# Optimization experiments

Measured on AMD Instinct MI355X. Metric: run time of the kernel, lower is better.

The kernel has to match this reference:

```python
import jax, jax.numpy as jnp
import numpy as np

# config
B, V, S, D = 2, 8, 256, 2048
NH, NKV, KVR = 32, 8, 2
HD = D // NH            # 64
G = NH // NKV           # GQA group size = 4
INIT = 0.02


def _neighbor_idx():
    # replicates generate_neighbor: left neighbors (i-half..i-1) then right (i+1..i+half), circular
    half = KVR // 2
    offsets = np.concatenate([np.arange(-half, 0), np.arange(1, half + 1)])
    return (np.arange(V)[:, None] + offsets[None, :]) % V  # [V, KVR]


def setup_inputs() -> dict:
    key = jax.random.key(0)
    k1, k2, k3, k4 = jax.random.split(key, 4)
    x = jax.random.normal(k1, (B, V, S, D), jnp.float32)
    wq = jax.random.normal(k2, (D, NH * HD), jnp.float32) * INIT
    wkv = jax.random.normal(k3, (D, 2 * NKV * HD), jnp.float32) * INIT
    wo = jax.random.normal(k4, (D, D), jnp.float32) * INIT
    return {"x": x, "wq": wq, "wkv": wkv, "wo": wo}


def reference(x, wq, wkv, wo):
    b, v, s, d = x.shape
    idx = _neighbor_idx()  # [V, KVR] static

    # Q projection: [b, v, s, NH*HD]
    xq = (x @ wq).reshape(b, v, s, NKV, G, HD)  # grouped-query layout (kv head, group)

    # neighbor gather: [b, v, KVR, s, d] -> [b, v, KVR*s, d]
    x_kv = x[:, idx].reshape(b, v, KVR * s, d)
    kv = x_kv @ wkv
    xk, xv = jnp.split(kv, 2, axis=-1)
    xk = xk.reshape(b, v, KVR * s, NKV, HD)
    xv = xv.reshape(b, v, KVR * s, NKV, HD)

    # grouped-query SDPA (no mask, eval mode): avoids materializing repeated K/V
    scale = 1.0 / jnp.sqrt(jnp.asarray(HD, x.dtype))
    scores = jnp.einsum('bvsngh,bvtnh->bvngst', xq, xk) * scale  # [b,v,NKV,G,s,KVR*s]
    attn = jax.nn.softmax(scores, axis=-1)
    out = jnp.einsum('bvngst,bvtnh->bvsngh', attn, xv).reshape(b, v, s, d)
    return out @ wo
```

## Files before the change

kernel.cpp:

```cpp
#include <hip/hip_runtime.h>
#include <stdint.h>

typedef unsigned short u16;
typedef unsigned int   u32;
typedef short short8 __attribute__((ext_vector_type(8)));
typedef float f32x4  __attribute__((ext_vector_type(4)));

__device__ __forceinline__ u16 f2bf(float f){
  u32 u = __builtin_bit_cast(u32, f);
  u32 r = (u + 0x7FFFu + ((u >> 16) & 1u)) >> 16;
  return (u16)r;
}
__device__ __forceinline__ u32 packbf(float a, float b){
  return (u32)f2bf(a) | ((u32)f2bf(b) << 16);
}
__device__ __forceinline__ void gload16(const u16* g, u16* l){
  __builtin_amdgcn_global_load_lds((const __attribute__((address_space(1))) void*)g,
                                   (__attribute__((address_space(3))) void*)l, 16, 0, 0);
}

__global__ __launch_bounds__(256) void k_cvt_bf16(const float* __restrict__ x,
                                                  u16* __restrict__ y, int n8){
  int i = blockIdx.x * 256 + threadIdx.x;
  if (i >= n8) return;
  const float4* p = (const float4*)x + (size_t)i * 2;
  float4 a = p[0], b = p[1];
  short8 o;
  o[0] = f2bf(a.x); o[1] = f2bf(a.y); o[2] = f2bf(a.z); o[3] = f2bf(a.w);
  o[4] = f2bf(b.x); o[5] = f2bf(b.y); o[6] = f2bf(b.z); o[7] = f2bf(b.w);
  *(short8*)(y + (size_t)i * 8) = o;
}

__global__ __launch_bounds__(256) void k_transpose_w(const float* __restrict__ in,
                                                     u16* __restrict__ out, int R, int C){
  __shared__ float tile[32][33];
  int nc = C >> 5;
  int cb = blockIdx.x % nc, rb = blockIdx.x / nc;
  int tx = threadIdx.x & 31, ty = threadIdx.x >> 5;
#pragma unroll
  for (int i = 0; i < 4; ++i){
    int r = rb * 32 + ty + i * 8;
    tile[ty + i * 8][tx] = in[(size_t)r * C + cb * 32 + tx];
  }
  __syncthreads();
#pragma unroll
  for (int i = 0; i < 4; ++i){
    int c = cb * 32 + ty + i * 8;
    out[(size_t)c * R + rb * 32 + tx] = f2bf(tile[tx][ty + i * 8]);
  }
}

template<int BN, int NFRAG, int BLOADS, typename CT>
__global__ __launch_bounds__(512, 2) void k_gemm8p(const u16* __restrict__ A,
                                                   const u16* __restrict__ Bt,
                                                   CT* __restrict__ C,
                                                   int N, int K){
  constexpr int SZA = 256 * 128;
  constexpr int SZB = BN * 128;
  constexpr int SZ  = SZA + SZB;
  constexpr int WT_N = BN / 4;
  __shared__ char lds[2 * SZ];

  int tid = threadIdx.x, lane = tid & 63, wid = tid >> 6;
  int l16 = lane & 15, g4 = lane >> 4;
  int wm = wid >> 2, wn = wid & 3;
  int bid = blockIdx.x;
  int wg = (bid & 7) * 32 + (bid >> 3);
  int bm = wg >> 4, bn = wg & 15;

  const u16* baseA = A  + (size_t)(bm * 256) * K;
  const u16* baseB = Bt + (size_t)(bn * BN) * K;

  int aLds[4], aG[4];
#pragma unroll
  for (int i = 0; i < 4; ++i){
    int q = (wid * 4 + i) * 1024 + lane * 16;
    int row = q >> 7, c = q & 127;
    int cs = c ^ ((row & 7) << 4);
    aLds[i] = q; aG[i] = row * K + (cs >> 1);
  }
  int bLds[BLOADS], bG[BLOADS];
#pragma unroll
  for (int j = 0; j < BLOADS; ++j){
    int q = (wid * BLOADS + j) * 1024 + lane * 16;
    int row = q >> 7, c = q & 127;
    int cs = c ^ ((row & 7) << 4);
    bLds[j] = q; bG[j] = row * K + (cs >> 1);
  }
  auto stageA = [&](int t){
    char* dst = lds + (t & 1) * SZ;
#pragma unroll
    for (int i = 0; i < 4; ++i) gload16(baseA + aG[i] + t * 64, (u16*)(dst + aLds[i]));
  };
  auto stageB = [&](int t){
    char* dst = lds + (t & 1) * SZ + SZA;
#pragma unroll
    for (int j = 0; j < BLOADS; ++j) gload16(baseB + bG[j] + t * 64, (u16*)(dst + bLds[j]));
  };
  auto rdA = [&](const char* Ab, int m, int ks){
    int row = wm * 128 + m * 16 + l16;
    return *(const short8*)(Ab + row * 128 + ((ks * 64 + g4 * 16) ^ ((row & 7) << 4)));
  };
  auto rdB = [&](const char* Bb, int nf, int ks){
    int row = wn * WT_N + nf * 16 + l16;
    return *(const short8*)(Bb + row * 128 + ((ks * 64 + g4 * 16) ^ ((row & 7) << 4)));
  };

  f32x4 zero4 = {0.f, 0.f, 0.f, 0.f};
  f32x4 acc[8][NFRAG];
#pragma unroll
  for (int i = 0; i < 8; ++i)
#pragma unroll
    for (int j = 0; j < NFRAG; ++j) acc[i][j] = zero4;

  int NK = K >> 6;
  stageA(0); stageB(0);
  asm volatile("s_waitcnt vmcnt(0)" ::: "memory");

  for (int kt = 0; kt < NK; ++kt){
    const char* Ab = lds + (kt & 1) * SZ;
    const char* Bb = Ab + SZA;
    bool st = (kt + 1 < NK);
    __builtin_amdgcn_s_barrier();
    short8 bf0[NFRAG], a0[4], a1[4], bf1[NFRAG], a2[4], a3[4];
#pragma unroll
    for (int nf = 0; nf < NFRAG; ++nf) bf0[nf] = rdB(Bb, nf, 0);
#pragma unroll
    for (int m = 0; m < 4; ++m) a0[m] = rdA(Ab, m, 0);
    if (st) stageA(kt + 1);
#pragma unroll
    for (int m = 0; m < 4; ++m) a1[m] = rdA(Ab, 4 + m, 0);
    __builtin_amdgcn_s_setprio(1);
#pragma unroll
    for (int m = 0; m < 4; ++m)
#pragma unroll
      for (int nf = 0; nf < NFRAG; ++nf)
        acc[m][nf] = __builtin_amdgcn_mfma_f32_16x16x32_bf16(a0[m], bf0[nf], acc[m][nf], 0, 0, 0);
    __builtin_amdgcn_s_setprio(0);
    __builtin_amdgcn_s_barrier();
    if (st) stageB(kt + 1);
#pragma unroll
    for (int nf = 0; nf < NFRAG; ++nf) bf1[nf] = rdB(Bb, nf, 1);
#pragma unroll
    for (int m = 0; m < 4; ++m) a2[m] = rdA(Ab, m, 1);
    __builtin_amdgcn_s_setprio(1);
#pragma unroll
    for (int m = 0; m < 4; ++m)
#pragma unroll
      for (int nf = 0; nf < NFRAG; ++nf)
        acc[4 + m][nf] = __builtin_amdgcn_mfma_f32_16x16x32_bf16(a1[m], bf0[nf], acc[4 + m][nf], 0, 0, 0);
    __builtin_amdgcn_s_setprio(0);
    __builtin_amdgcn_s_barrier();
#pragma unroll
    for (int m = 0; m < 4; ++m) a3[m] = rdA(Ab, 4 + m, 1);
    __builtin_amdgcn_s_setprio(1);
#pragma unroll
    for (int m = 0; m < 4; ++m)
#pragma unroll
      for (int nf = 0; nf < NFRAG; ++nf)
        acc[m][nf] = __builtin_amdgcn_mfma_f32_16x16x32_bf16(a2[m], bf1[nf], acc[m][nf], 0, 0, 0);
    __builtin_amdgcn_s_setprio(0);
    __builtin_amdgcn_s_barrier();
    __builtin_amdgcn_s_setprio(1);
#pragma unroll
    for (int m = 0; m < 4; ++m)
#pragma unroll
      for (int nf = 0; nf < NFRAG; ++nf)
        acc[4 + m][nf] = __builtin_amdgcn_mfma_f32_16x16x32_bf16(a3[m], bf1[nf], acc[4 + m][nf], 0, 0, 0);
    __builtin_amdgcn_s_setprio(0);
    if (st) asm volatile("s_waitcnt vmcnt(0)" ::: "memory");
  }

#pragma unroll
  for (int mf = 0; mf < 8; ++mf)
#pragma unroll
    for (int nf = 0; nf < NFRAG; ++nf)
#pragma unroll
      for (int r = 0; r < 4; ++r){
        int row = bm * 256 + wm * 128 + mf * 16 + g4 * 4 + r;
        int col = bn * BN + wn * WT_N + nf * 16 + l16;
        float vv = acc[mf][nf][r];
        if constexpr (sizeof(CT) == 2) C[(size_t)row * N + col] = (CT)f2bf(vv);
        else                           C[(size_t)row * N + col] = (CT)vv;
      }
}

__global__ __launch_bounds__(256) void k_vt(const u16* __restrict__ c1, u16* __restrict__ vt){
  __shared__ u16 tile[64][72];
  int bid = blockIdx.x;
  int st = bid & 3, n = (bid >> 2) & 7, bv = bid >> 5;
  int t = threadIdx.x;
  int sr = t >> 2, sc = t & 3;
  const u16* src = c1 + (size_t)(bv * 256 + st * 64 + sr) * 3072 + 2560 + n * 64 + sc * 16;
  short8 a = *(const short8*)src;
  short8 b = *(const short8*)(src + 8);
  *(short8*)&tile[sr][sc * 16]     = a;
  *(short8*)&tile[sr][sc * 16 + 8] = b;
  __syncthreads();
  int h = t >> 2, c2 = t & 3;
  short8 o0, o1;
#pragma unroll
  for (int j = 0; j < 8; ++j) o0[j] = (short)tile[c2 * 16 + j][h];
#pragma unroll
  for (int j = 0; j < 8; ++j) o1[j] = (short)tile[c2 * 16 + 8 + j][h];
  u16* dst = vt + (size_t)((bv * 8 + n) * 64 + h) * 256 + st * 64 + c2 * 16;
  *(short8*)dst       = o0;
  *(short8*)(dst + 8) = o1;
}

__global__ __launch_bounds__(256, 2) void k_attn(const u16* __restrict__ c1,
                                                 const u16* __restrict__ vt,
                                                 u16* __restrict__ att){
  __shared__ u16 Klds[64][72];
  __shared__ u16 Vlds[64][72];
  __shared__ u16 Plds[4][16][72];
  int bid = blockIdx.x;
  int qt = bid & 3, n = (bid >> 2) & 7, v = (bid >> 5) & 7, b = bid >> 8;
  int tid = threadIdx.x;
  int g = tid >> 6, lane = tid & 63, l16 = lane & 15, g4 = lane >> 4;
  int bv = b * 8 + v;
  int rowQ = bv * 256 + qt * 64;
  int qcol = n * 256 + g * 64;
  const float SC2 = 0.18033688011112042f;

  short8 qf[4][2];
#pragma unroll
  for (int qi = 0; qi < 4; ++qi)
#pragma unroll
    for (int kk = 0; kk < 2; ++kk)
      qf[qi][kk] = *(const short8*)(c1 + (size_t)(rowQ + qi * 16 + l16) * 3072
                                     + qcol + kk * 32 + g4 * 8);

  f32x4 zero4 = {0.f, 0.f, 0.f, 0.f};
  f32x4 O[4][4];
#pragma unroll
  for (int i = 0; i < 4; ++i)
#pragma unroll
    for (int j = 0; j < 4; ++j) O[i][j] = zero4;
  float m2[4]   = {-3.0e38f, -3.0e38f, -3.0e38f, -3.0e38f};
  float lsum[4] = {0.f, 0.f, 0.f, 0.f};

  int sr = tid >> 2, sc = tid & 3;
  short8 k0, k1, v0, v1;
  {
    int vn = (v + 7) & 7;
    const u16* ks = c1 + (size_t)((b * 8 + vn) * 256 + sr) * 3072 + 2048 + n * 64 + sc * 16;
    k0 = *(const short8*)ks; k1 = *(const short8*)(ks + 8);
    const u16* vs = vt + (size_t)(((b * 8 + vn) * 8 + n) * 64 + sr) * 256 + sc * 16;
    v0 = *(const short8*)vs; v1 = *(const short8*)(vs + 8);
  }

  for (int ti = 0; ti < 8; ++ti){
    __syncthreads();
    *(short8*)&Klds[sr][sc * 16]     = k0;
    *(short8*)&Klds[sr][sc * 16 + 8] = k1;
    *(short8*)&Vlds[sr][sc * 16]     = v0;
    *(short8*)&Vlds[sr][sc * 16 + 8] = v1;
    __syncthreads();
    if (ti < 7){
      int tn = ti + 1;
      int vn = (tn < 4) ? ((v + 7) & 7) : ((v + 1) & 7);
      int tb = (tn & 3) * 64;
      const u16* ks = c1 + (size_t)((b * 8 + vn) * 256 + tb + sr) * 3072 + 2048 + n * 64 + sc * 16;
      k0 = *(const short8*)ks; k1 = *(const short8*)(ks + 8);
      const u16* vs = vt + (size_t)(((b * 8 + vn) * 8 + n) * 64 + sr) * 256 + tb + sc * 16;
      v0 = *(const short8*)vs; v1 = *(const short8*)(vs + 8);
    }
    short8 kf[4][2], vf[2][4];
#pragma unroll
    for (int kt = 0; kt < 4; ++kt)
#pragma unroll
      for (int ks = 0; ks < 2; ++ks)
        kf[kt][ks] = *(const short8*)&Klds[kt * 16 + l16][ks * 32 + g4 * 8];
#pragma unroll
    for (int ks = 0; ks < 2; ++ks)
#pragma unroll
      for (int hi = 0; hi < 4; ++hi)
        vf[ks][hi] = *(const short8*)&Vlds[hi * 16 + l16][ks * 32 + g4 * 8];

#pragma unroll
    for (int qi = 0; qi < 4; ++qi){
      f32x4 sa[4];
#pragma unroll
      for (int kt = 0; kt < 4; ++kt){
        sa[kt] = zero4;
#pragma unroll
        for (int ks = 0; ks < 2; ++ks)
          sa[kt] = __builtin_amdgcn_mfma_f32_16x16x32_bf16(kf[kt][ks], qf[qi][ks], sa[kt], 0, 0, 0);
      }
      float smax = -3.0e38f;
#pragma unroll
      for (int kt = 0; kt < 4; ++kt)
#pragma unroll
        for (int r = 0; r < 4; ++r){
          float s = sa[kt][r] * SC2;
          sa[kt][r] = s;
          smax = fmaxf(smax, s);
        }
      smax = fmaxf(smax, __shfl_xor(smax, 16));
      smax = fmaxf(smax, __shfl_xor(smax, 32));
      float mnew  = fmaxf(m2[qi], smax);
      float alpha = exp2f(m2[qi] - mnew);
      m2[qi] = mnew;
      float psum = 0.f;
      u32 w[4][2];
#pragma unroll
      for (int kt = 0; kt < 4; ++kt){
        float p0 = exp2f(sa[kt][0] - mnew);
        float p1 = exp2f(sa[kt][1] - mnew);
        float p2 = exp2f(sa[kt][2] - mnew);
        float p3 = exp2f(sa[kt][3] - mnew);
        psum += (p0 + p1) + (p2 + p3);
        w[kt][0] = packbf(p0, p1);
        w[kt][1] = packbf(p2, p3);
      }
      psum += __shfl_xor(psum, 16);
      psum += __shfl_xor(psum, 32);
      lsum[qi] = lsum[qi] * alpha + psum;
      u32* prow = (u32*)&Plds[g][l16][0];
#pragma unroll
      for (int kt = 0; kt < 4; ++kt){
        prow[kt * 8 + g4 * 2]     = w[kt][0];
        prow[kt * 8 + g4 * 2 + 1] = w[kt][1];
      }
      float ab[4];
#pragma unroll
      for (int r = 0; r < 4; ++r) ab[r] = __shfl(alpha, g4 * 4 + r);
#pragma unroll
      for (int hi = 0; hi < 4; ++hi)
#pragma unroll
        for (int r = 0; r < 4; ++r) O[qi][hi][r] *= ab[r];
      short8 pa[2];
#pragma unroll
      for (int ks = 0; ks < 2; ++ks)
        pa[ks] = *(const short8*)&Plds[g][l16][ks * 32 + g4 * 8];
#pragma unroll
      for (int hi = 0; hi < 4; ++hi)
#pragma unroll
        for (int ks = 0; ks < 2; ++ks)
          O[qi][hi] = __builtin_amdgcn_mfma_f32_16x16x32_bf16(pa[ks], vf[ks][hi], O[qi][hi], 0, 0, 0);
    }
  }
#pragma unroll
  for (int qi = 0; qi < 4; ++qi){
    float lb[4];
#pragma unroll
    for (int r = 0; r < 4; ++r) lb[r] = 1.0f / __shfl(lsum[qi], g4 * 4 + r);
#pragma unroll
    for (int hi = 0; hi < 4; ++hi)
#pragma unroll
      for (int r = 0; r < 4; ++r){
        int row = rowQ + qi * 16 + g4 * 4 + r;
        int col = qcol + hi * 16 + l16;
        att[(size_t)row * 2048 + col] = f2bf(O[qi][hi][r] * lb[r]);
      }
  }
}

extern "C" void kernel_launch(void* const* d_in, const int* in_sizes, int n_in,
                              void* d_out, int out_size, void* d_ws, size_t ws_size,
                              hipStream_t stream){
  const float* x   = (const float*)d_in[0];
  const float* wq  = (const float*)d_in[1];
  const float* wkv = (const float*)d_in[2];
  const float* wo  = (const float*)d_in[3];
  float* out = (float*)d_out;
  char* ws = (char*)d_ws;

  u16* x_bf  = (u16*)(ws);
  u16* wqkvt = (u16*)(ws + 16777216);
  u16* wot   = (u16*)(ws + 29360128);
  u16* c1    = (u16*)(ws + 37748736);
  u16* vt    = (u16*)(ws + 62914560);
  u16* att   = x_bf;

  k_cvt_bf16<<<4096, 256, 0, stream>>>(x, x_bf, 1048576);
  k_transpose_w<<<4096, 256, 0, stream>>>(wq,  wqkvt,               2048, 2048);
  k_transpose_w<<<2048, 256, 0, stream>>>(wkv, wqkvt + 2048 * 2048, 2048, 1024);
  k_transpose_w<<<4096, 256, 0, stream>>>(wo,  wot,                 2048, 2048);
  k_gemm8p<192, 3, 3, u16><<<256, 512, 0, stream>>>(x_bf, wqkvt, c1, 3072, 2048);
  k_vt<<<512, 256, 0, stream>>>(c1, vt);
  k_attn<<<512, 256, 0, stream>>>(c1, vt, att);
  k_gemm8p<128, 2, 2, float><<<256, 512, 0, stream>>>(att, wot, out, 2048, 2048);
}
```

Baseline: 160.6 us.

## Fold softmax scale into Q GEMM, lazy rescale, smaller attention tiles, new output GEMM

The softmax scale (times log2 e) is now applied to the Q columns in the QKV GEMM epilogue, so the attention loop no longer multiplies scores. Attention tiles shrink to 32 query rows per block with 1024 blocks and a higher occupancy bound. The online softmax only rescales O and the running sum when the running max grows by more than 8, and bf16 packing uses the hardware v_cvt_pk_bf16_f32 instruction. The output projection moves to a new 128x256-tile GEMM with a 3-stage LDS pipeline. The risks are lower K/V reuse per block and bf16 precision loss, because lazy rescaling can let exp2 values reach 256.

After: 210.9 us. +31.3%, slower.

```diff
diff --git a/kernel.cpp b/kernel.cpp
--- a/kernel.cpp
+++ b/kernel.cpp
@@ -11,8 +11,8 @@
   u32 r = (u + 0x7FFFu + ((u >> 16) & 1u)) >> 16;
   return (u16)r;
 }
-__device__ __forceinline__ u32 packbf(float a, float b){
-  return (u32)f2bf(a) | ((u32)f2bf(b) << 16);
+__device__ __forceinline__ u32 cvtpk(float a, float b){
+  u32 r; asm("v_cvt_pk_bf16_f32 %0, %1, %2" : "=v"(r) : "v"(a), "v"(b)); return r;
 }
 __device__ __forceinline__ void gload16(const u16* g, u16* l){
   __builtin_amdgcn_global_load_lds((const __attribute__((address_space(1))) void*)g,
@@ -50,7 +50,7 @@
   }
 }
 
-template<int BN, int NFRAG, int BLOADS, typename CT>
+template<int BN, int NFRAG, int BLOADS, bool QSCALE, typename CT>
 __global__ __launch_bounds__(512, 2) void k_gemm8p(const u16* __restrict__ A,
                                                    const u16* __restrict__ Bt,
                                                    CT* __restrict__ C,
@@ -180,8 +180,119 @@
         int row = bm * 256 + wm * 128 + mf * 16 + g4 * 4 + r;
         int col = bn * BN + wn * WT_N + nf * 16 + l16;
         float vv = acc[mf][nf][r];
+        if constexpr (QSCALE) { if (col < 2048) vv *= 0.18033688011112042f; }
         if constexpr (sizeof(CT) == 2) C[(size_t)row * N + col] = (CT)f2bf(vv);
         else                           C[(size_t)row * N + col] = (CT)vv;
+      }
+}
+
+__global__ __launch_bounds__(512, 1) void k_gemm_o(const u16* __restrict__ A,
+                                                   const u16* __restrict__ Bt,
+                                                   float* __restrict__ C,
+                                                   int N, int K){
+  constexpr int SZA = 128 * 128;
+  constexpr int SZB = 256 * 128;
+  constexpr int SZ  = SZA + SZB;
+  __shared__ char lds[3 * SZ];
+
+  int tid = threadIdx.x, lane = tid & 63, wid = tid >> 6;
+  int l16 = lane & 15, g4 = lane >> 4;
+  int wm = wid >> 2, wn = wid & 3;
+  int bid = blockIdx.x;
+  int wg = (bid & 7) * 32 + (bid >> 3);
+  int bm = wg >> 3, bn = wg & 7;
+
+  const u16* baseA = A  + (size_t)(bm * 128) * K;
+  const u16* baseB = Bt + (size_t)(bn * 256) * K;
+
+  int aLds[2], aG[2];
+#pragma unroll
+  for (int i = 0; i < 2; ++i){
+    int q = (wid * 2 + i) * 1024 + lane * 16;
+    int row = q >> 7, c = q & 127;
+    int cs = c ^ ((row & 7) << 4);
+    aLds[i] = q; aG[i] = row * K + (cs >> 1);
+  }
+  int bLds[4], bG[4];
+#pragma unroll
+  for (int j = 0; j < 4; ++j){
+    int q = (wid * 4 + j) * 1024 + lane * 16;
+    int row = q >> 7, c = q & 127;
+    int cs = c ^ ((row & 7) << 4);
+    bLds[j] = q; bG[j] = row * K + (cs >> 1);
+  }
+  auto stage = [&](int t, int buf){
+    char* dst = lds + buf * SZ;
+#pragma unroll
+    for (int i = 0; i < 2; ++i) gload16(baseA + aG[i] + t * 64, (u16*)(dst + aLds[i]));
+#pragma unroll
+    for (int j = 0; j < 4; ++j) gload16(baseB + bG[j] + t * 64, (u16*)(dst + SZA + bLds[j]));
+  };
+  auto rdA = [&](const char* Ab, int m, int ks){
+    int row = wm * 64 + m * 16 + l16;
+    return *(const short8*)(Ab + row * 128 + ((ks * 64 + g4 * 16) ^ ((row & 7) << 4)));
+  };
+  auto rdB = [&](const char* Bb, int nf, int ks){
+    int row = wn * 64 + nf * 16 + l16;
+    return *(const short8*)(Bb + row * 128 + ((ks * 64 + g4 * 16) ^ ((row & 7) << 4)));
+  };
+
+  f32x4 zero4 = {0.f, 0.f, 0.f, 0.f};
+  f32x4 acc[4][4];
+#pragma unroll
+  for (int i = 0; i < 4; ++i)
+#pragma unroll
+    for (int j = 0; j < 4; ++j) acc[i][j] = zero4;
+
+  int NK = K >> 6;
+  stage(0, 0); stage(1, 1);
+  int cur = 0, stb = 2;
+
+  for (int kt = 0; kt < NK; ++kt){
+    if (kt + 1 < NK) asm volatile("s_waitcnt vmcnt(6)" ::: "memory");
+    else             asm volatile("s_waitcnt vmcnt(0)" ::: "memory");
+    __builtin_amdgcn_s_barrier();
+    __builtin_amdgcn_sched_barrier(0);
+
+    const char* Ab = lds + cur * SZ;
+    const char* Bb = Ab + SZA;
+
+    short8 bf0[4], a0[4], bf1[4], a1[4];
+#pragma unroll
+    for (int nf = 0; nf < 4; ++nf) bf0[nf] = rdB(Bb, nf, 0);
+#pragma unroll
+    for (int m = 0; m < 4; ++m)    a0[m]  = rdA(Ab, m, 0);
+    if (kt + 2 < NK) stage(kt + 2, stb);
+#pragma unroll
+    for (int nf = 0; nf < 4; ++nf) bf1[nf] = rdB(Bb, nf, 1);
+#pragma unroll
+    for (int m = 0; m < 4; ++m)    a1[m]  = rdA(Ab, m, 1);
+    __builtin_amdgcn_s_setprio(1);
+#pragma unroll
+    for (int m = 0; m < 4; ++m)
+#pragma unroll
+      for (int nf = 0; nf < 4; ++nf)
+        acc[m][nf] = __builtin_amdgcn_mfma_f32_16x16x32_bf16(a0[m], bf0[nf], acc[m][nf], 0, 0, 0);
+#pragma unroll
+    for (int m = 0; m < 4; ++m)
+#pragma unroll
+      for (int nf = 0; nf < 4; ++nf)
+        acc[m][nf] = __builtin_amdgcn_mfma_f32_16x16x32_bf16(a1[m], bf1[nf], acc[m][nf], 0, 0, 0);
+    __builtin_amdgcn_s_setprio(0);
+
+    cur = (cur == 2) ? 0 : cur + 1;
+    stb = (stb == 2) ? 0 : stb + 1;
+  }
+
+#pragma unroll
+  for (int mf = 0; mf < 4; ++mf)
+#pragma unroll
+    for (int nf = 0; nf < 4; ++nf)
+#pragma unroll
+      for (int r = 0; r < 4; ++r){
+        int row = bm * 128 + wm * 64 + mf * 16 + g4 * 4 + r;
+        int col = bn * 256 + wn * 64 + nf * 16 + l16;
+        C[(size_t)row * N + col] = acc[mf][nf][r];
       }
 }
 
@@ -208,37 +319,36 @@
   *(short8*)(dst + 8) = o1;
 }
 
-__global__ __launch_bounds__(256, 2) void k_attn(const u16* __restrict__ c1,
+__global__ __launch_bounds__(256, 4) void k_attn(const u16* __restrict__ c1,
                                                  const u16* __restrict__ vt,
                                                  u16* __restrict__ att){
   __shared__ u16 Klds[64][72];
   __shared__ u16 Vlds[64][72];
   __shared__ u16 Plds[4][16][72];
   int bid = blockIdx.x;
-  int qt = bid & 3, n = (bid >> 2) & 7, v = (bid >> 5) & 7, b = bid >> 8;
+  int qt = bid & 7, n = (bid >> 3) & 7, v = (bid >> 6) & 7, b = bid >> 9;
   int tid = threadIdx.x;
   int g = tid >> 6, lane = tid & 63, l16 = lane & 15, g4 = lane >> 4;
   int bv = b * 8 + v;
-  int rowQ = bv * 256 + qt * 64;
+  int rowQ = bv * 256 + qt * 32;
   int qcol = n * 256 + g * 64;
-  const float SC2 = 0.18033688011112042f;
-
-  short8 qf[4][2];
-#pragma unroll
-  for (int qi = 0; qi < 4; ++qi)
+
+  short8 qf[2][2];
+#pragma unroll
+  for (int qi = 0; qi < 2; ++qi)
 #pragma unroll
     for (int kk = 0; kk < 2; ++kk)
       qf[qi][kk] = *(const short8*)(c1 + (size_t)(rowQ + qi * 16 + l16) * 3072
                                      + qcol + kk * 32 + g4 * 8);
 
   f32x4 zero4 = {0.f, 0.f, 0.f, 0.f};
-  f32x4 O[4][4];
-#pragma unroll
-  for (int i = 0; i < 4; ++i)
+  f32x4 O[2][4];
+#pragma unroll
+  for (int i = 0; i < 2; ++i)
 #pragma unroll
     for (int j = 0; j < 4; ++j) O[i][j] = zero4;
-  float m2[4]   = {-3.0e38f, -3.0e38f, -3.0e38f, -3.0e38f};
-  float lsum[4] = {0.f, 0.f, 0.f, 0.f};
+  float m2[2]   = {-3.0e38f, -3.0e38f};
+  float lsum[2] = {0.f, 0.f};
 
   int sr = tid >> 2, sc = tid & 3;
   short8 k0, k1, v0, v1;
@@ -279,7 +389,7 @@
         vf[ks][hi] = *(const short8*)&Vlds[hi * 16 + l16][ks * 32 + g4 * 8];
 
 #pragma unroll
-    for (int qi = 0; qi < 4; ++qi){
+    for (int qi = 0; qi < 2; ++qi){
       f32x4 sa[4];
 #pragma unroll
       for (int kt = 0; kt < 4; ++kt){
@@ -288,48 +398,48 @@
         for (int ks = 0; ks < 2; ++ks)
           sa[kt] = __builtin_amdgcn_mfma_f32_16x16x32_bf16(kf[kt][ks], qf[qi][ks], sa[kt], 0, 0, 0);
       }
-      float smax = -3.0e38f;
+      float pmax = sa[0][0];
 #pragma unroll
       for (int kt = 0; kt < 4; ++kt)
 #pragma unroll
-        for (int r = 0; r < 4; ++r){
-          float s = sa[kt][r] * SC2;
-          sa[kt][r] = s;
-          smax = fmaxf(smax, s);
-        }
-      smax = fmaxf(smax, __shfl_xor(smax, 16));
-      smax = fmaxf(smax, __shfl_xor(smax, 32));
-      float mnew  = fmaxf(m2[qi], smax);
-      float alpha = exp2f(m2[qi] - mnew);
-      m2[qi] = mnew;
+        for (int r = 0; r < 4; ++r) pmax = fmaxf(pmax, sa[kt][r]);
+      pmax = fmaxf(pmax, __shfl_xor(pmax, 16));
+      pmax = fmaxf(pmax, __shfl_xor(pmax, 32));
+      if (__any(pmax > m2[qi] + 8.f)){
+        float mnew  = fmaxf(m2[qi], pmax);
+        float alpha = exp2f(m2[qi] - mnew);
+        m2[qi] = mnew;
+        lsum[qi] *= alpha;
+        float ab[4];
+#pragma unroll
+        for (int r = 0; r < 4; ++r) ab[r] = __shfl(alpha, g4 * 4 + r);
+#pragma unroll
+        for (int hi = 0; hi < 4; ++hi)
+#pragma unroll
+          for (int r = 0; r < 4; ++r) O[qi][hi][r] *= ab[r];
+      }
+      float m = m2[qi];
       float psum = 0.f;
       u32 w[4][2];
 #pragma unroll
       for (int kt = 0; kt < 4; ++kt){
-        float p0 = exp2f(sa[kt][0] - mnew);
-        float p1 = exp2f(sa[kt][1] - mnew);
-        float p2 = exp2f(sa[kt][2] - mnew);
-        float p3 = exp2f(sa[kt][3] - mnew);
+        float p0 = exp2f(sa[kt][0] - m);
+        float p1 = exp2f(sa[kt][1] - m);
+        float p2 = exp2f(sa[kt][2] - m);
+        float p3 = exp2f(sa[kt][3] - m);
         psum += (p0 + p1) + (p2 + p3);
-        w[kt][0] = packbf(p0, p1);
-        w[kt][1] = packbf(p2, p3);
+        w[kt][0] = cvtpk(p0, p1);
+        w[kt][1] = cvtpk(p2, p3);
       }
       psum += __shfl_xor(psum, 16);
       psum += __shfl_xor(psum, 32);
-      lsum[qi] = lsum[qi] * alpha + psum;
+      lsum[qi] += psum;
       u32* prow = (u32*)&Plds[g][l16][0];
 #pragma unroll
       for (int kt = 0; kt < 4; ++kt){
         prow[kt * 8 + g4 * 2]     = w[kt][0];
         prow[kt * 8 + g4 * 2 + 1] = w[kt][1];
       }
-      float ab[4];
-#pragma unroll
-      for (int r = 0; r < 4; ++r) ab[r] = __shfl(alpha, g4 * 4 + r);
-#pragma unroll
-      for (int hi = 0; hi < 4; ++hi)
-#pragma unroll
-        for (int r = 0; r < 4; ++r) O[qi][hi][r] *= ab[r];
       short8 pa[2];
 #pragma unroll
       for (int ks = 0; ks < 2; ++ks)
@@ -342,7 +452,7 @@
     }
   }
 #pragma unroll
-  for (int qi = 0; qi < 4; ++qi){
+  for (int qi = 0; qi < 2; ++qi){
     float lb[4];
 #pragma unroll
     for (int r = 0; r < 4; ++r) lb[r] = 1.0f / __shfl(lsum[qi], g4 * 4 + r);
@@ -378,8 +488,8 @@
   k_transpose_w<<<4096, 256, 0, stream>>>(wq,  wqkvt,               2048, 2048);
   k_transpose_w<<<2048, 256, 0, stream>>>(wkv, wqkvt + 2048 * 2048, 2048, 1024);
   k_transpose_w<<<4096, 256, 0, stream>>>(wo,  wot,                 2048, 2048);
-  k_gemm8p<192, 3, 3, u16><<<256, 512, 0, stream>>>(x_bf, wqkvt, c1, 3072, 2048);
+  k_gemm8p<192, 3, 3, true, u16><<<256, 512, 0, stream>>>(x_bf, wqkvt, c1, 3072, 2048);
   k_vt<<<512, 256, 0, stream>>>(c1, vt);
-  k_attn<<<512, 256, 0, stream>>>(c1, vt, att);
-  k_gemm8p<128, 2, 2, float><<<256, 512, 0, stream>>>(att, wot, out, 2048, 2048);
-}
+  k_attn<<<1024, 256, 0, stream>>>(c1, vt, att);
+  k_gemm_o<<<256, 512, 0, stream>>>(att, wot, out, 2048, 2048);
+}
```

## Software-pipeline GEMM LDS reads, fold Q scale into projection, lazy softmax rescale

Applied to the files above, without the earlier changes.

The GEMM now prefetches the next k-tile's first fragments across the barrier and places scheduling barriers around each phase. It is also templated on BM, which changes the output GEMM tile to 128x256 and launch bounds to one block per CU. The softmax scale is folded into the Q columns in the QKV GEMM epilogue. Attention rescales the running max only when it grows by more than 8, skipping the exp and O rescale otherwise, and uses the hardware packed bf16 convert. These cut per-iteration overhead in both GEMMs and attention, at the cost of lower occupancy and slightly different rounding.

Measured after the change: 154.7 us. 1.04x faster.

```diff
diff --git a/kernel.cpp b/kernel.cpp
--- a/kernel.cpp
+++ b/kernel.cpp
@@ -11,13 +11,14 @@
   u32 r = (u + 0x7FFFu + ((u >> 16) & 1u)) >> 16;
   return (u16)r;
 }
-__device__ __forceinline__ u32 packbf(float a, float b){
-  return (u32)f2bf(a) | ((u32)f2bf(b) << 16);
+__device__ __forceinline__ u32 cvtpk(float a, float b){
+  u32 r; asm("v_cvt_pk_bf16_f32 %0, %1, %2" : "=v"(r) : "v"(a), "v"(b)); return r;
 }
 __device__ __forceinline__ void gload16(const u16* g, u16* l){
   __builtin_amdgcn_global_load_lds((const __attribute__((address_space(1))) void*)g,
                                    (__attribute__((address_space(3))) void*)l, 16, 0, 0);
 }
+#define BARRIER()  do{ __builtin_amdgcn_s_barrier(); __builtin_amdgcn_sched_barrier(0); }while(0)
 
 __global__ __launch_bounds__(256) void k_cvt_bf16(const float* __restrict__ x,
                                                   u16* __restrict__ y, int n8){
@@ -50,15 +51,16 @@
   }
 }
 
-template<int BN, int NFRAG, int BLOADS, typename CT>
-__global__ __launch_bounds__(512, 2) void k_gemm8p(const u16* __restrict__ A,
+template<int BM, int BN, int MH, int NFRAG, int ALOADS, int BLOADS, bool QSCALE, typename CT>
+__global__ __launch_bounds__(512, 1) void k_gemm8p(const u16* __restrict__ A,
                                                    const u16* __restrict__ Bt,
                                                    CT* __restrict__ C,
                                                    int N, int K){
-  constexpr int SZA = 256 * 128;
+  constexpr int SZA = BM * 128;
   constexpr int SZB = BN * 128;
   constexpr int SZ  = SZA + SZB;
-  constexpr int WT_N = BN / 4;
+  constexpr int WTM = BM / 2;
+  constexpr int WTN = BN / 4;
   __shared__ char lds[2 * SZ];
 
   int tid = threadIdx.x, lane = tid & 63, wid = tid >> 6;
@@ -66,15 +68,16 @@
   int wm = wid >> 2, wn = wid & 3;
   int bid = blockIdx.x;
   int wg = (bid & 7) * 32 + (bid >> 3);
-  int bm = wg >> 4, bn = wg & 15;
-
-  const u16* baseA = A  + (size_t)(bm * 256) * K;
+  int nb = N / BN;
+  int bm = wg / nb, bn = wg % nb;
+
+  const u16* baseA = A  + (size_t)(bm * BM) * K;
   const u16* baseB = Bt + (size_t)(bn * BN) * K;
 
-  int aLds[4], aG[4];
-#pragma unroll
-  for (int i = 0; i < 4; ++i){
-    int q = (wid * 4 + i) * 1024 + lane * 16;
+  int aLds[ALOADS], aG[ALOADS];
+#pragma unroll
+  for (int i = 0; i < ALOADS; ++i){
+    int q = (wid * ALOADS + i) * 1024 + lane * 16;
     int row = q >> 7, c = q & 127;
     int cs = c ^ ((row & 7) << 4);
     aLds[i] = q; aG[i] = row * K + (cs >> 1);
@@ -90,7 +93,7 @@
   auto stageA = [&](int t){
     char* dst = lds + (t & 1) * SZ;
 #pragma unroll
-    for (int i = 0; i < 4; ++i) gload16(baseA + aG[i] + t * 64, (u16*)(dst + aLds[i]));
+    for (int i = 0; i < ALOADS; ++i) gload16(baseA + aG[i] + t * 64, (u16*)(dst + aLds[i]));
   };
   auto stageB = [&](int t){
     char* dst = lds + (t & 1) * SZ + SZA;
@@ -98,88 +101,99 @@
     for (int j = 0; j < BLOADS; ++j) gload16(baseB + bG[j] + t * 64, (u16*)(dst + bLds[j]));
   };
   auto rdA = [&](const char* Ab, int m, int ks){
-    int row = wm * 128 + m * 16 + l16;
+    int row = wm * WTM + m * 16 + l16;
     return *(const short8*)(Ab + row * 128 + ((ks * 64 + g4 * 16) ^ ((row & 7) << 4)));
   };
   auto rdB = [&](const char* Bb, int nf, int ks){
-    int row = wn * WT_N + nf * 16 + l16;
+    int row = wn * WTN + nf * 16 + l16;
     return *(const short8*)(Bb + row * 128 + ((ks * 64 + g4 * 16) ^ ((row & 7) << 4)));
   };
 
   f32x4 zero4 = {0.f, 0.f, 0.f, 0.f};
-  f32x4 acc[8][NFRAG];
-#pragma unroll
-  for (int i = 0; i < 8; ++i)
+  f32x4 acc[2 * MH][NFRAG];
+#pragma unroll
+  for (int i = 0; i < 2 * MH; ++i)
 #pragma unroll
     for (int j = 0; j < NFRAG; ++j) acc[i][j] = zero4;
 
   int NK = K >> 6;
   stageA(0); stageB(0);
   asm volatile("s_waitcnt vmcnt(0)" ::: "memory");
+  BARRIER();
+  short8 a0[MH], a1[MH], a2[MH], a3[MH], bf0[NFRAG], bf1[NFRAG];
+#pragma unroll
+  for (int nf = 0; nf < NFRAG; ++nf) bf0[nf] = rdB(lds + SZA, nf, 0);
+#pragma unroll
+  for (int m = 0; m < MH; ++m)       a0[m]  = rdA(lds, m, 0);
 
   for (int kt = 0; kt < NK; ++kt){
     const char* Ab = lds + (kt & 1) * SZ;
     const char* Bb = Ab + SZA;
     bool st = (kt + 1 < NK);
-    __builtin_amdgcn_s_barrier();
-    short8 bf0[NFRAG], a0[4], a1[4], bf1[NFRAG], a2[4], a3[4];
-#pragma unroll
-    for (int nf = 0; nf < NFRAG; ++nf) bf0[nf] = rdB(Bb, nf, 0);
-#pragma unroll
-    for (int m = 0; m < 4; ++m) a0[m] = rdA(Ab, m, 0);
+#pragma unroll
+    for (int m = 0; m < MH; ++m) a1[m] = rdA(Ab, MH + m, 0);
     if (st) stageA(kt + 1);
-#pragma unroll
-    for (int m = 0; m < 4; ++m) a1[m] = rdA(Ab, 4 + m, 0);
+    BARRIER();
     __builtin_amdgcn_s_setprio(1);
 #pragma unroll
-    for (int m = 0; m < 4; ++m)
+    for (int m = 0; m < MH; ++m)
 #pragma unroll
       for (int nf = 0; nf < NFRAG; ++nf)
         acc[m][nf] = __builtin_amdgcn_mfma_f32_16x16x32_bf16(a0[m], bf0[nf], acc[m][nf], 0, 0, 0);
     __builtin_amdgcn_s_setprio(0);
-    __builtin_amdgcn_s_barrier();
+#pragma unroll
+    for (int nf = 0; nf < NFRAG; ++nf) bf1[nf] = rdB(Bb, nf, 1);
+#pragma unroll
+    for (int m = 0; m < MH; ++m)       a2[m]  = rdA(Ab, m, 1);
     if (st) stageB(kt + 1);
-#pragma unroll
-    for (int nf = 0; nf < NFRAG; ++nf) bf1[nf] = rdB(Bb, nf, 1);
-#pragma unroll
-    for (int m = 0; m < 4; ++m) a2[m] = rdA(Ab, m, 1);
+    BARRIER();
     __builtin_amdgcn_s_setprio(1);
 #pragma unroll
-    for (int m = 0; m < 4; ++m)
+    for (int m = 0; m < MH; ++m)
 #pragma unroll
       for (int nf = 0; nf < NFRAG; ++nf)
-        acc[4 + m][nf] = __builtin_amdgcn_mfma_f32_16x16x32_bf16(a1[m], bf0[nf], acc[4 + m][nf], 0, 0, 0);
+        acc[MH + m][nf] = __builtin_amdgcn_mfma_f32_16x16x32_bf16(a1[m], bf0[nf], acc[MH + m][nf], 0, 0, 0);
     __builtin_amdgcn_s_setprio(0);
-    __builtin_amdgcn_s_barrier();
-#pragma unroll
-    for (int m = 0; m < 4; ++m) a3[m] = rdA(Ab, 4 + m, 1);
+#pragma unroll
+    for (int m = 0; m < MH; ++m) a3[m] = rdA(Ab, MH + m, 1);
+    BARRIER();
     __builtin_amdgcn_s_setprio(1);
 #pragma unroll
-    for (int m = 0; m < 4; ++m)
+    for (int m = 0; m < MH; ++m)
 #pragma unroll
       for (int nf = 0; nf < NFRAG; ++nf)
         acc[m][nf] = __builtin_amdgcn_mfma_f32_16x16x32_bf16(a2[m], bf1[nf], acc[m][nf], 0, 0, 0);
     __builtin_amdgcn_s_setprio(0);
-    __builtin_amdgcn_s_barrier();
+    if (st) asm volatile("s_waitcnt vmcnt(0)" ::: "memory");
+    BARRIER();
+    if (st){
+      const char* Ab2 = lds + ((kt + 1) & 1) * SZ;
+      const char* Bb2 = Ab2 + SZA;
+#pragma unroll
+      for (int nf = 0; nf < NFRAG; ++nf) bf0[nf] = rdB(Bb2, nf, 0);
+#pragma unroll
+      for (int m = 0; m < MH; ++m)       a0[m]  = rdA(Ab2, m, 0);
+    }
     __builtin_amdgcn_s_setprio(1);
 #pragma unroll
-    for (int m = 0; m < 4; ++m)
+    for (int m = 0; m < MH; ++m)
 #pragma unroll
       for (int nf = 0; nf < NFRAG; ++nf)
-        acc[4 + m][nf] = __builtin_amdgcn_mfma_f32_16x16x32_bf16(a3[m], bf1[nf], acc[4 + m][nf], 0, 0, 0);
+        acc[MH + m][nf] = __builtin_amdgcn_mfma_f32_16x16x32_bf16(a3[m], bf1[nf], acc[MH + m][nf], 0, 0, 0);
     __builtin_amdgcn_s_setprio(0);
-    if (st) asm volatile("s_waitcnt vmcnt(0)" ::: "memory");
-  }
-
-#pragma unroll
-  for (int mf = 0; mf < 8; ++mf)
+    BARRIER();
+  }
+
+#pragma unroll
+  for (int mf = 0; mf < 2 * MH; ++mf)
 #pragma unroll
     for (int nf = 0; nf < NFRAG; ++nf)
 #pragma unroll
       for (int r = 0; r < 4; ++r){
-        int row = bm * 256 + wm * 128 + mf * 16 + g4 * 4 + r;
-        int col = bn * BN + wn * WT_N + nf * 16 + l16;
+        int row = bm * BM + wm * WTM + mf * 16 + g4 * 4 + r;
+        int col = bn * BN + wn * WTN + nf * 16 + l16;
         float vv = acc[mf][nf][r];
+        if constexpr (QSCALE) { if (col < 2048) vv *= 0.18033688011112042f; }
         if constexpr (sizeof(CT) == 2) C[(size_t)row * N + col] = (CT)f2bf(vv);
         else                           C[(size_t)row * N + col] = (CT)vv;
       }
@@ -221,7 +235,6 @@
   int bv = b * 8 + v;
   int rowQ = bv * 256 + qt * 64;
   int qcol = n * 256 + g * 64;
-  const float SC2 = 0.18033688011112042f;
 
   short8 qf[4][2];
 #pragma unroll
@@ -288,48 +301,48 @@
         for (int ks = 0; ks < 2; ++ks)
           sa[kt] = __builtin_amdgcn_mfma_f32_16x16x32_bf16(kf[kt][ks], qf[qi][ks], sa[kt], 0, 0, 0);
       }
-      float smax = -3.0e38f;
+      float pmax = sa[0][0];
 #pragma unroll
       for (int kt = 0; kt < 4; ++kt)
 #pragma unroll
-        for (int r = 0; r < 4; ++r){
-          float s = sa[kt][r] * SC2;
-          sa[kt][r] = s;
-          smax = fmaxf(smax, s);
-        }
-      smax = fmaxf(smax, __shfl_xor(smax, 16));
-      smax = fmaxf(smax, __shfl_xor(smax, 32));
-      float mnew  = fmaxf(m2[qi], smax);
-      float alpha = exp2f(m2[qi] - mnew);
-      m2[qi] = mnew;
+        for (int r = 0; r < 4; ++r) pmax = fmaxf(pmax, sa[kt][r]);
+      pmax = fmaxf(pmax, __shfl_xor(pmax, 16));
+      pmax = fmaxf(pmax, __shfl_xor(pmax, 32));
+      if (__any(pmax > m2[qi] + 8.f)){
+        float mnew  = fmaxf(m2[qi], pmax);
+        float alpha = exp2f(m2[qi] - mnew);
+        m2[qi] = mnew;
+        lsum[qi] *= alpha;
+        float ab[4];
+#pragma unroll
+        for (int r = 0; r < 4; ++r) ab[r] = __shfl(alpha, g4 * 4 + r);
+#pragma unroll
+        for (int hi = 0; hi < 4; ++hi)
+#pragma unroll
+          for (int r = 0; r < 4; ++r) O[qi][hi][r] *= ab[r];
+      }
+      float m = m2[qi];
       float psum = 0.f;
       u32 w[4][2];
 #pragma unroll
       for (int kt = 0; kt < 4; ++kt){
-        float p0 = exp2f(sa[kt][0] - mnew);
-        float p1 = exp2f(sa[kt][1] - mnew);
-        float p2 = exp2f(sa[kt][2] - mnew);
-        float p3 = exp2f(sa[kt][3] - mnew);
+        float p0 = exp2f(sa[kt][0] - m);
+        float p1 = exp2f(sa[kt][1] - m);
+        float p2 = exp2f(sa[kt][2] - m);
+        float p3 = exp2f(sa[kt][3] - m);
         psum += (p0 + p1) + (p2 + p3);
-        w[kt][0] = packbf(p0, p1);
-        w[kt][1] = packbf(p2, p3);
+        w[kt][0] = cvtpk(p0, p1);
+        w[kt][1] = cvtpk(p2, p3);
       }
       psum += __shfl_xor(psum, 16);
       psum += __shfl_xor(psum, 32);
-      lsum[qi] = lsum[qi] * alpha + psum;
+      lsum[qi] += psum;
       u32* prow = (u32*)&Plds[g][l16][0];
 #pragma unroll
       for (int kt = 0; kt < 4; ++kt){
         prow[kt * 8 + g4 * 2]     = w[kt][0];
         prow[kt * 8 + g4 * 2 + 1] = w[kt][1];
       }
-      float ab[4];
-#pragma unroll
-      for (int r = 0; r < 4; ++r) ab[r] = __shfl(alpha, g4 * 4 + r);
-#pragma unroll
-      for (int hi = 0; hi < 4; ++hi)
-#pragma unroll
-        for (int r = 0; r < 4; ++r) O[qi][hi][r] *= ab[r];
       short8 pa[2];
 #pragma unroll
       for (int ks = 0; ks < 2; ++ks)
@@ -378,8 +391,8 @@
   k_transpose_w<<<4096, 256, 0, stream>>>(wq,  wqkvt,               2048, 2048);
   k_transpose_w<<<2048, 256, 0, stream>>>(wkv, wqkvt + 2048 * 2048, 2048, 1024);
   k_transpose_w<<<4096, 256, 0, stream>>>(wo,  wot,                 2048, 2048);
-  k_gemm8p<192, 3, 3, u16><<<256, 512, 0, stream>>>(x_bf, wqkvt, c1, 3072, 2048);
+  k_gemm8p<256, 192, 4, 3, 4, 3, true,  u16  ><<<256, 512, 0, stream>>>(x_bf, wqkvt, c1, 3072, 2048);
   k_vt<<<512, 256, 0, stream>>>(c1, vt);
   k_attn<<<512, 256, 0, stream>>>(c1, vt, att);
-  k_gemm8p<128, 2, 2, float><<<256, 512, 0, stream>>>(att, wot, out, 2048, 2048);
-}
+  k_gemm8p<128, 256, 2, 4, 2, 4, false, float><<<256, 512, 0, stream>>>(att, wot, out, 2048, 2048);
+}
```
